# Kernel optimization log

Measured on AMD Instinct MI355X. Metric: run time of the kernel, lower is better.

Reference implementation:

```python
import jax, jax.numpy as jnp
import numpy as np

S, D, A, H, C = 2048, 256, 64, 8, 64  # seq_len, node_dim, num_aux, num_heads, num_channels
QUAT = 4
N_TYPES = 3  # nodes, aux, rot


def _linear_params(key, out_dim, in_dim, use_bias=True):
    kw, kb = jax.random.split(key)
    lim = 1.0 / np.sqrt(in_dim)
    W = jax.random.uniform(kw, (out_dim, in_dim), minval=-lim, maxval=lim, dtype=jnp.float32)
    if not use_bias:
        return W, None
    b = jax.random.uniform(kb, (out_dim,), minval=-lim, maxval=lim, dtype=jnp.float32)
    return W, b


def setup_inputs() -> dict:
    key = jax.random.key(0)
    ks = jax.random.split(key, 8)
    nodes = jax.random.normal(ks[0], (S, D), dtype=jnp.float32)
    aux = jax.random.normal(ks[1], (S, A), dtype=jnp.float32)
    rot = jax.random.normal(ks[2], (S, QUAT), dtype=jnp.float32)
    W_nodes, b_nodes = _linear_params(ks[3], H * C * 2, D)
    W_aux, b_aux = _linear_params(ks[4], H * C * 2, A)
    W_rot, _ = _linear_params(ks[5], H * C * 2, QUAT, use_bias=False)
    W_val, b_val = _linear_params(ks[6], D * H * N_TYPES, D)
    return {
        "nodes": nodes, "aux": aux, "rot": rot,
        "W_nodes": W_nodes, "b_nodes": b_nodes,
        "W_aux": W_aux, "b_aux": b_aux,
        "W_rot": W_rot,
        "W_val": W_val, "b_val": b_val,
    }


def reference(nodes, aux, rot, W_nodes, b_nodes, W_aux, b_aux, W_rot, W_val, b_val):
    seq_len = nodes.shape[0]
    # values: (S, 3H, D)
    val = (nodes @ W_val.T + b_val).reshape(seq_len, N_TYPES * H, -1)
    # per-source k/q: each (S, H, C)
    nodes_k, nodes_q = jnp.split((nodes @ W_nodes.T + b_nodes).reshape(seq_len, H, -1), 2, -1)
    aux_k, aux_q = jnp.split((aux @ W_aux.T + b_aux).reshape(seq_len, H, -1), 2, -1)
    rot_k, rot_q = jnp.split((rot @ W_rot.T).reshape(seq_len, H, -1), 2, -1)
    # concat along head axis -> (S, 3H, C)
    k = jnp.concatenate([nodes_k, aux_k, rot_k], axis=-2)
    q = jnp.concatenate([nodes_q, aux_q, rot_q], axis=-2)
    # (S, S, 3H) score tensor, scaled by 1/sqrt(num_heads) as in the original
    logits = jnp.einsum('ihc,jhc->ijh', k, q) / jnp.sqrt(jnp.asarray(H, nodes.dtype))
    att = jax.nn.softmax(logits, axis=-2)  # softmax over the j (key) axis
    out = jnp.einsum('ijh,jhd->id', att, val)  # (S, D)
    return out
```

## Files before the change

### kernel.cpp

```cpp
#include <hip/hip_runtime.h>

#define S_LEN 2048
#define NHEAD 24
#define CDIM 64
#define DDIM 256

typedef _Float16 f16x8 __attribute__((ext_vector_type(8)));
typedef float f32x4 __attribute__((ext_vector_type(4)));

__device__ __forceinline__ ushort f2h(float f) {
    _Float16 h = (_Float16)f;
    return __builtin_bit_cast(ushort, h);
}
__device__ __forceinline__ uint pkh(float a, float b) {
    auto v = __builtin_amdgcn_cvt_pkrtz(a, b);
    return __builtin_bit_cast(uint, v);
}
__device__ __forceinline__ uint pk2(float a, float b) {
    return (uint)f2h(a) | ((uint)f2h(b) << 16);
}

__device__ __forceinline__ int4 cvt8(const float* __restrict__ p) {
    float4 a = *(const float4*)p;
    float4 b = *(const float4*)(p + 4);
    f16x8 h;
    h[0] = (_Float16)a.x; h[1] = (_Float16)a.y;
    h[2] = (_Float16)a.z; h[3] = (_Float16)a.w;
    h[4] = (_Float16)b.x; h[5] = (_Float16)b.y;
    h[6] = (_Float16)b.z; h[7] = (_Float16)b.w;
    return __builtin_bit_cast(int4, h);
}

#define SCALE_K 0.51006973f

__global__ __launch_bounds__(256) void prep_kernel(
    const float* __restrict__ nodes, const float* __restrict__ W_val,
    float* __restrict__ out, ushort* __restrict__ nodes16, ushort* __restrict__ Wval16)
{
    int idx = blockIdx.x * 256 + threadIdx.x;
    if (idx < 131072) {
        ((float4*)out)[idx] = float4{0.f, 0.f, 0.f, 0.f};
    } else if (idx < 196608) {
        int i = idx - 131072;
        *(int4*)&nodes16[i * 8] = cvt8(&nodes[i * 8]);
    } else {
        int i = idx - 196608;
        *(int4*)&Wval16[i * 8] = cvt8(&W_val[i * 8]);
    }
}

__global__ __launch_bounds__(256) void proj_kernel(
    const float* __restrict__ nodes, const float* __restrict__ W_nodes,
    const float* __restrict__ b_nodes,
    const float* __restrict__ aux, const float* __restrict__ W_aux,
    const float* __restrict__ b_aux,
    const float* __restrict__ rot, const float* __restrict__ W_rot,
    const ushort* __restrict__ nodes16, const ushort* __restrict__ Wval16,
    const float* __restrict__ b_val,
    ushort* __restrict__ Kbuf, ushort* __restrict__ Qbuf, ushort* __restrict__ Vt)
{
    __shared__ ushort Asub[128 * 72];
    __shared__ ushort Wsub[128 * 72];
    const int blk = blockIdx.x;
    const int tid = threadIdx.x;
    const int wave = tid >> 6, lane = tid & 63;
    const int g = lane >> 4, c = lane & 15;

    if (blk < 768) {
        const int wm = wave & 1, wn = wave >> 1;
        const int m0 = (blk / 48) * 128, n0 = (blk % 48) * 128;
        const int K = 256;

        f32x4 acc[16];
#pragma unroll
        for (int t = 0; t < 16; t++) acc[t] = f32x4{0, 0, 0, 0};

        for (int k0 = 0; k0 < K; k0 += 64) {
            __syncthreads();
#pragma unroll
            for (int q = 0; q < 4; q++) {
                int i = tid + 256 * q;
                int row = i >> 3, kc = (i & 7) * 8;
                *(int4*)&Asub[row * 72 + kc] = *(const int4*)&nodes16[(m0 + row) * K + k0 + kc];
                *(int4*)&Wsub[row * 72 + kc] = *(const int4*)&Wval16[(n0 + row) * K + k0 + kc];
            }
            __syncthreads();

            f16x8 af0[4], af1[4];
#pragma unroll
            for (int mt = 0; mt < 4; mt++) {
                const ushort* Ar = &Asub[(wm * 64 + mt * 16 + c) * 72 + g * 8];
                af0[mt] = *(const f16x8*)Ar;
                af1[mt] = *(const f16x8*)(Ar + 32);
            }
#pragma unroll
            for (int nt = 0; nt < 4; nt++) {
                const ushort* Wr = &Wsub[(wn * 64 + nt * 16 + c) * 72 + g * 8];
                f16x8 bf0 = *(const f16x8*)Wr;
                f16x8 bf1 = *(const f16x8*)(Wr + 32);
#pragma unroll
                for (int mt = 0; mt < 4; mt++) {
                    acc[mt * 4 + nt] = __builtin_amdgcn_mfma_f32_16x16x32_f16(af0[mt], bf0, acc[mt * 4 + nt], 0, 0, 0);
                    acc[mt * 4 + nt] = __builtin_amdgcn_mfma_f32_16x16x32_f16(af1[mt], bf1, acc[mt * 4 + nt], 0, 0, 0);
                }
            }
        }

#pragma unroll
        for (int nt = 0; nt < 4; nt++) {
            int n = n0 + wn * 64 + nt * 16 + c;
            float bv = b_val[n];
            int h = n >> 8, d = n & 255;
#pragma unroll
            for (int mt = 0; mt < 4; mt++) {
                int m = m0 + wm * 64 + mt * 16 + g * 4;
                f32x4 v = acc[mt * 4 + nt];
                uint2 pw;
                pw.x = pk2(v[0] + bv, v[1] + bv);
                pw.y = pk2(v[2] + bv, v[3] + bv);
                *(uint2*)&Vt[(h * DDIM + d) * S_LEN + m] = pw;
            }
        }
    } else if (blk < 1792) {
        const int sub = blk - 768;
        const float *A, *W, *b;
        int K, hbase;
        if (sub < 512) { A = nodes; W = W_nodes; b = b_nodes; K = 256; hbase = 0; }
        else           { A = aux;   W = W_aux;   b = b_aux;   K = 64;  hbase = 8; }
        const int t5 = sub & 511;
        const int m0 = (t5 >> 4) * 64, n0 = (t5 & 15) * 64;
        const int srow = tid >> 2;
        const int skk = (tid & 3) * 8;

        f32x4 acc[4] = {f32x4{0,0,0,0}, f32x4{0,0,0,0}, f32x4{0,0,0,0}, f32x4{0,0,0,0}};

        for (int k0 = 0; k0 < K; k0 += 32) {
            __syncthreads();
            *(int4*)&Asub[srow * 40 + skk] = cvt8(&A[(m0 + srow) * K + k0 + skk]);
            *(int4*)&Wsub[srow * 40 + skk] = cvt8(&W[(n0 + srow) * K + k0 + skk]);
            __syncthreads();
            f16x8 af = *(const f16x8*)&Asub[(wave * 16 + c) * 40 + g * 8];
#pragma unroll
            for (int t = 0; t < 4; t++) {
                f16x8 bf = *(const f16x8*)&Wsub[(t * 16 + c) * 40 + g * 8];
                acc[t] = __builtin_amdgcn_mfma_f32_16x16x32_f16(af, bf, acc[t], 0, 0, 0);
            }
        }

#pragma unroll
        for (int t = 0; t < 4; t++) {
            int n = n0 + t * 16 + c;
            float bv = b[n];
            int h = hbase + (n >> 7);
            int cc = n & 127;
            float sc = (cc < 64) ? SCALE_K : 1.0f;
#pragma unroll
            for (int r = 0; r < 4; r++) {
                int m = m0 + wave * 16 + g * 4 + r;
                ushort u = f2h((acc[t][r] + bv) * sc);
                if (cc < 64) Kbuf[(h * S_LEN + m) * CDIM + cc] = u;
                else         Qbuf[(h * S_LEN + m) * CDIM + cc - 64] = u;
            }
        }
    } else {
        int u = (blk - 1792) * 256 + tid;
        int i = u >> 7;
        int n8 = (u & 127) * 8;
        int cc = n8 & 127;
        float sc = (cc < 64) ? SCALE_K : 1.0f;
        float4 r = *(const float4*)&rot[i * 4];
        ushort pv[8];
#pragma unroll
        for (int q = 0; q < 8; q++) {
            float4 w = *(const float4*)&W_rot[(n8 + q) * 4];
            pv[q] = f2h((r.x * w.x + r.y * w.y + r.z * w.z + r.w * w.w) * sc);
        }
        int h = 16 + (n8 >> 7);
        int4 pkt = *(int4*)pv;
        if (cc < 64) *(int4*)&Kbuf[(h * S_LEN + i) * CDIM + cc] = pkt;
        else         *(int4*)&Qbuf[(h * S_LEN + i) * CDIM + cc - 64] = pkt;
    }
}

__global__ __launch_bounds__(256, 3) void flash_kernel(
    const ushort* __restrict__ Kbuf, const ushort* __restrict__ Qbuf,
    const ushort* __restrict__ Vt, float* __restrict__ out)
{
    __shared__ ushort Qlds[2][64 * 72];
    __shared__ ushort Plds[2][64 * 72];
    __shared__ float  Alds[2][64];
    __shared__ int    Need[2][4] __attribute__((aligned(16)));

    const int tid = threadIdx.x;
    const int wave = tid >> 6, lane = tid & 63;
    const int g = lane >> 4, c = lane & 15;
    const int lin = blockIdx.y * 32 + blockIdx.x;
    const int xcd = lin & 7;
    const int slot = lin >> 3;
    const int h = xcd * 3 + (slot >> 5);
    const int i0 = (slot & 31) * 64;
    const float THR = 8.0f;

    const ushort* Krow = &Kbuf[(h * S_LEN + i0 + wave * 16 + c) * CDIM + g * 8];
    f16x8 ka0 = *(const f16x8*)Krow;
    f16x8 ka1 = *(const f16x8*)(Krow + 32);

    const ushort* Vbase = &Vt[(h * DDIM + wave * 64 + c) * S_LEN + g * 8];
    const ushort* Qh = &Qbuf[h * S_LEN * CDIM];

    const int qr0 = tid >> 3, qc0 = (tid & 7) * 8;
    const int qr1 = qr0 + 32;

    *(int4*)&Qlds[0][qr0 * 72 + qc0] = *(const int4*)&Qh[qr0 * CDIM + qc0];
    *(int4*)&Qlds[0][qr1 * 72 + qc0] = *(const int4*)&Qh[qr1 * CDIM + qc0];
    int4 qn0 = *(const int4*)&Qh[(64 + qr0) * CDIM + qc0];
    int4 qn1 = *(const int4*)&Qh[(64 + qr1) * CDIM + qc0];

    f16x8 vf0[4], vf1[4];
#pragma unroll
    for (int u = 0; u < 4; u++) {
        const ushort* Vr = Vbase + (u * 16) * S_LEN;
        vf0[u] = *(const f16x8*)Vr;
        vf1[u] = *(const f16x8*)(Vr + 32);
    }

    f32x4 acc[16];
#pragma unroll
    for (int u = 0; u < 16; u++) acc[u] = f32x4{0, 0, 0, 0};
    float mrow = -1e30f, lrow = 0.f;

    __syncthreads();

    {
        f32x4 Sf[4];
#pragma unroll
        for (int jc = 0; jc < 4; jc++) {
            const ushort* Qr = &Qlds[0][(jc * 16 + c) * 72 + g * 8];
            f16x8 qb0 = *(const f16x8*)Qr;
            f16x8 qb1 = *(const f16x8*)(Qr + 32);
            f32x4 s = {0, 0, 0, 0};
            s = __builtin_amdgcn_mfma_f32_16x16x32_f16(qb0, ka0, s, 0, 0, 0);
            s = __builtin_amdgcn_mfma_f32_16x16x32_f16(qb1, ka1, s, 0, 0, 0);
            Sf[jc] = s;
        }
        float tm = -1e30f;
#pragma unroll
        for (int jc = 0; jc < 4; jc++)
            tm = fmaxf(tm, fmaxf(fmaxf(Sf[jc][0], Sf[jc][1]),
                                 fmaxf(Sf[jc][2], Sf[jc][3])));
        tm = fmaxf(tm, __shfl_xor(tm, 16));
        tm = fmaxf(tm, __shfl_xor(tm, 32));
        const bool need = __any(tm > mrow + THR);
        float nm, alpha;
        if (need) { nm = fmaxf(tm, mrow); alpha = exp2f(mrow - nm); }
        else      { nm = mrow; alpha = 1.0f; }
        if (lane == 0) Need[0][wave] = need ? 1 : 0;
        float rs = 0.f;
#pragma unroll
        for (int jc = 0; jc < 4; jc++) {
            float p0 = exp2f(Sf[jc][0] - nm);
            float p1 = exp2f(Sf[jc][1] - nm);
            float p2 = exp2f(Sf[jc][2] - nm);
            float p3 = exp2f(Sf[jc][3] - nm);
            rs += (p0 + p1) + (p2 + p3);
            uint2 w;
            w.x = pkh(p0, p1);
            w.y = pkh(p2, p3);
            *(uint2*)&Plds[0][(wave * 16 + c) * 72 + jc * 16 + g * 4] = w;
        }
        lrow = lrow * alpha + rs;
        mrow = nm;
        if (g == 0) Alds[0][wave * 16 + c] = alpha;
    }
    *(int4*)&Qlds[1][qr0 * 72 + qc0] = qn0;
    *(int4*)&Qlds[1][qr1 * 72 + qc0] = qn1;

    for (int t = 0; t < 31; ++t) {
        const int cur = t & 1, nxt = cur ^ 1;
        __syncthreads();

        if (t < 30) {
            qn0 = *(const int4*)&Qh[((t + 2) * 64 + qr0) * CDIM + qc0];
            qn1 = *(const int4*)&Qh[((t + 2) * 64 + qr1) * CDIM + qc0];
        }

        f32x4 Sf[4];
#pragma unroll
        for (int jc = 0; jc < 4; jc++) {
            const ushort* Qr = &Qlds[nxt][(jc * 16 + c) * 72 + g * 8];
            f16x8 qb0 = *(const f16x8*)Qr;
            f16x8 qb1 = *(const f16x8*)(Qr + 32);
            f32x4 s = {0, 0, 0, 0};
            s = __builtin_amdgcn_mfma_f32_16x16x32_f16(qb0, ka0, s, 0, 0, 0);
            s = __builtin_amdgcn_mfma_f32_16x16x32_f16(qb1, ka1, s, 0, 0, 0);
            Sf[jc] = s;
        }

        int4 nf = *(const int4*)&Need[cur][0];
        if (nf.x | nf.y | nf.z | nf.w) {
#pragma unroll
            for (int b = 0; b < 4; b++) {
                f32x4 ab = *(const f32x4*)&Alds[cur][b * 16 + g * 4];
#pragma unroll
                for (int u = 0; u < 4; u++) acc[b * 4 + u] *= ab;
            }
        }

#pragma unroll
        for (int b = 0; b < 4; b++) {
            const ushort* Pr = &Plds[cur][(b * 16 + c) * 72 + g * 8];
            f16x8 pa0 = *(const f16x8*)Pr;
            f16x8 pa1 = *(const f16x8*)(Pr + 32);
#pragma unroll
            for (int u = 0; u < 4; u++) {
                acc[b * 4 + u] = __builtin_amdgcn_mfma_f32_16x16x32_f16(pa0, vf0[u], acc[b * 4 + u], 0, 0, 0);
                acc[b * 4 + u] = __builtin_amdgcn_mfma_f32_16x16x32_f16(pa1, vf1[u], acc[b * 4 + u], 0, 0, 0);
            }
        }

#pragma unroll
        for (int u = 0; u < 4; u++) {
            const ushort* Vr = Vbase + (u * 16) * S_LEN + (t + 1) * 64;
            vf0[u] = *(const f16x8*)Vr;
            vf1[u] = *(const f16x8*)(Vr + 32);
        }

        {
            float tl = -1e30f;
#pragma unroll
            for (int jc = 0; jc < 4; jc++)
                tl = fmaxf(tl, fmaxf(fmaxf(Sf[jc][0], Sf[jc][1]),
                                     fmaxf(Sf[jc][2], Sf[jc][3])));
            const bool need = __any(tl > mrow + THR);
            float nm, alpha;
            if (need) {
                float tm = fmaxf(tl, __shfl_xor(tl, 16));
                tm = fmaxf(tm, __shfl_xor(tm, 32));
                nm = fmaxf(tm, mrow);
                alpha = exp2f(mrow - nm);
            } else { nm = mrow; alpha = 1.0f; }
            if (lane == 0) Need[nxt][wave] = need ? 1 : 0;
            float rs = 0.f;
#pragma unroll
            for (int jc = 0; jc < 4; jc++) {
                float p0 = exp2f(Sf[jc][0] - nm);
                float p1 = exp2f(Sf[jc][1] - nm);
                float p2 = exp2f(Sf[jc][2] - nm);
                float p3 = exp2f(Sf[jc][3] - nm);
                rs += (p0 + p1) + (p2 + p3);
                uint2 w;
                w.x = pkh(p0, p1);
                w.y = pkh(p2, p3);
                *(uint2*)&Plds[nxt][(wave * 16 + c) * 72 + jc * 16 + g * 4] = w;
            }
            lrow = lrow * alpha + rs;
            mrow = nm;
            if (g == 0) Alds[nxt][wave * 16 + c] = alpha;
        }

        if (t < 30) {
            *(int4*)&Qlds[cur][qr0 * 72 + qc0] = qn0;
            *(int4*)&Qlds[cur][qr1 * 72 + qc0] = qn1;
        }
    }

    __syncthreads();
    {
        int4 nf = *(const int4*)&Need[1][0];
        if (nf.x | nf.y | nf.z | nf.w) {
#pragma unroll
            for (int b = 0; b < 4; b++) {
                f32x4 ab = *(const f32x4*)&Alds[1][b * 16 + g * 4];
#pragma unroll
                for (int u = 0; u < 4; u++) acc[b * 4 + u] *= ab;
            }
        }
#pragma unroll
        for (int b = 0; b < 4; b++) {
            const ushort* Pr = &Plds[1][(b * 16 + c) * 72 + g * 8];
            f16x8 pa0 = *(const f16x8*)Pr;
            f16x8 pa1 = *(const f16x8*)(Pr + 32);
#pragma unroll
            for (int u = 0; u < 4; u++) {
                acc[b * 4 + u] = __builtin_amdgcn_mfma_f32_16x16x32_f16(pa0, vf0[u], acc[b * 4 + u], 0, 0, 0);
                acc[b * 4 + u] = __builtin_amdgcn_mfma_f32_16x16x32_f16(pa1, vf1[u], acc[b * 4 + u], 0, 0, 0);
            }
        }
    }

    lrow += __shfl_xor(lrow, 16);
    lrow += __shfl_xor(lrow, 32);

    __syncthreads();
    if (g == 0) Alds[0][wave * 16 + c] = 1.0f / lrow;
    __syncthreads();
#pragma unroll
    for (int b = 0; b < 4; b++) {
        f32x4 lb = *(const f32x4*)&Alds[0][b * 16 + g * 4];
#pragma unroll
        for (int u = 0; u < 4; u++)
#pragma unroll
            for (int r = 0; r < 4; r++) {
                int i = i0 + b * 16 + g * 4 + r;
                int d = wave * 64 + u * 16 + c;
                atomicAdd(&out[i * DDIM + d], acc[b * 4 + u][r] * lb[r]);
            }
    }
}

extern "C" void kernel_launch(void* const* d_in, const int* in_sizes, int n_in,
                              void* d_out, int out_size, void* d_ws, size_t ws_size,
                              hipStream_t stream) {
    const float *nodes = 0, *aux = 0, *rot = 0, *W_nodes = 0, *b_nodes = 0,
                *W_aux = 0, *b_aux = 0, *W_rot = 0, *W_val = 0, *b_val = 0;
    int i1024[2] = {-1, -1};
    int n1024 = 0;
    for (int i = 0; i < n_in; ++i) {
        const float* p = (const float*)d_in[i];
        switch (in_sizes[i]) {
            case 524288:  nodes   = p; break;
            case 131072:  aux     = p; break;
            case 8192:    rot     = p; break;
            case 262144:  W_nodes = p; break;
            case 65536:   W_aux   = p; break;
            case 4096:    W_rot   = p; break;
            case 1572864: W_val   = p; break;
            case 6144:    b_val   = p; break;
            case 1024:    if (n1024 < 2) i1024[n1024] = i; n1024++; break;
            default: break;
        }
    }
    if (n1024 == 2) {
        b_nodes = (const float*)d_in[i1024[0]];
        b_aux   = (const float*)d_in[i1024[1]];
    }
    if (!nodes || !aux || !rot || !W_nodes || !b_nodes || !W_aux || !b_aux ||
        !W_rot || !W_val || !b_val) {
        nodes   = (const float*)d_in[0];
        aux     = (const float*)d_in[1];
        rot     = (const float*)d_in[2];
        W_nodes = (const float*)d_in[3];
        b_nodes = (const float*)d_in[4];
        W_aux   = (const float*)d_in[5];
        b_aux   = (const float*)d_in[6];
        W_rot   = (const float*)d_in[7];
        W_val   = (const float*)d_in[8];
        b_val   = (const float*)d_in[9];
    }
    float* out = (float*)d_out;

    float*  Opad = (float*)d_ws;
    ushort* Kbuf = (ushort*)(Opad + S_LEN * DDIM);
    ushort* Qbuf = Kbuf + NHEAD * S_LEN * CDIM;
    ushort* Vt   = Qbuf + NHEAD * S_LEN * CDIM;
    ushort* nodes16 = Vt + NHEAD * DDIM * S_LEN;
    ushort* Wval16  = nodes16 + 524288;

    dim3 blk(256);
    prep_kernel<<<dim3(1536), blk, 0, stream>>>(nodes, W_val, out, nodes16, Wval16);
    proj_kernel<<<dim3(2816), blk, 0, stream>>>(
        nodes, W_nodes, b_nodes, aux, W_aux, b_aux, rot, W_rot,
        nodes16, Wval16, b_val, Kbuf, Qbuf, Vt);
    flash_kernel<<<dim3(32, NHEAD), blk, 0, stream>>>(Kbuf, Qbuf, Vt, out);
}
```

Baseline: 241.5 us.

## Load projection GEMM tiles directly to LDS with XOR swizzle; raise MFMA priority

The value-projection GEMM now stages A and W tiles through global_load_lds with an XOR-swizzled 64-wide row layout. This replaces register round-trip loads into padded 72-wide LDS rows and aims to cut VGPR traffic and bank conflicts. The attention loop also wraps its MFMA sections in s_setprio(1)/s_setprio(0), so waves issuing matrix ops get scheduling priority. The direct-to-LDS path depends on the per-lane address-to-LDS layout matching the swizzle, and the priority hints may give little benefit.

```diff
diff --git a/kernel.cpp b/kernel.cpp
--- a/kernel.cpp
+++ b/kernel.cpp
@@ -29,6 +29,12 @@
     h[4] = (_Float16)b.x; h[5] = (_Float16)b.y;
     h[6] = (_Float16)b.z; h[7] = (_Float16)b.w;
     return __builtin_bit_cast(int4, h);
+}
+
+__device__ __forceinline__ void gload16(const void* g, void* l) {
+    __builtin_amdgcn_global_load_lds(
+        (const __attribute__((address_space(1))) void*)g,
+        (__attribute__((address_space(3))) void*)l, 16, 0, 0);
 }
 
 #define SCALE_K 0.51006973f
@@ -70,6 +76,7 @@
         const int wm = wave & 1, wn = wave >> 1;
         const int m0 = (blk / 48) * 128, n0 = (blk % 48) * 128;
         const int K = 256;
+        const int x = c & 7;
 
         f32x4 acc[16];
 #pragma unroll
@@ -79,25 +86,27 @@
             __syncthreads();
 #pragma unroll
             for (int q = 0; q < 4; q++) {
-                int i = tid + 256 * q;
-                int row = i >> 3, kc = (i & 7) * 8;
-                *(int4*)&Asub[row * 72 + kc] = *(const int4*)&nodes16[(m0 + row) * K + k0 + kc];
-                *(int4*)&Wsub[row * 72 + kc] = *(const int4*)&Wval16[(n0 + row) * K + k0 + kc];
+                const int r0 = wave * 32 + q * 8;
+                const int row = r0 + (lane >> 3);
+                const int sl = lane & 7;
+                const int sc = ((sl ^ (row & 7)) * 8);
+                gload16(&nodes16[(m0 + row) * K + k0 + sc], &Asub[r0 * 64]);
+                gload16(&Wval16[(n0 + row) * K + k0 + sc], &Wsub[r0 * 64]);
             }
             __syncthreads();
 
             f16x8 af0[4], af1[4];
 #pragma unroll
             for (int mt = 0; mt < 4; mt++) {
-                const ushort* Ar = &Asub[(wm * 64 + mt * 16 + c) * 72 + g * 8];
-                af0[mt] = *(const f16x8*)Ar;
-                af1[mt] = *(const f16x8*)(Ar + 32);
+                const int row = wm * 64 + mt * 16 + c;
+                af0[mt] = *(const f16x8*)&Asub[row * 64 + ((g ^ x) * 8)];
+                af1[mt] = *(const f16x8*)&Asub[row * 64 + (((g + 4) ^ x) * 8)];
             }
 #pragma unroll
             for (int nt = 0; nt < 4; nt++) {
-                const ushort* Wr = &Wsub[(wn * 64 + nt * 16 + c) * 72 + g * 8];
-                f16x8 bf0 = *(const f16x8*)Wr;
-                f16x8 bf1 = *(const f16x8*)(Wr + 32);
+                const int row = wn * 64 + nt * 16 + c;
+                f16x8 bf0 = *(const f16x8*)&Wsub[row * 64 + ((g ^ x) * 8)];
+                f16x8 bf1 = *(const f16x8*)&Wsub[row * 64 + (((g + 4) ^ x) * 8)];
 #pragma unroll
                 for (int mt = 0; mt < 4; mt++) {
                     acc[mt * 4 + nt] = __builtin_amdgcn_mfma_f32_16x16x32_f16(af0[mt], bf0, acc[mt * 4 + nt], 0, 0, 0);
@@ -285,6 +294,7 @@
         }
 
         f32x4 Sf[4];
+        __builtin_amdgcn_s_setprio(1);
 #pragma unroll
         for (int jc = 0; jc < 4; jc++) {
             const ushort* Qr = &Qlds[nxt][(jc * 16 + c) * 72 + g * 8];
@@ -295,6 +305,7 @@
             s = __builtin_amdgcn_mfma_f32_16x16x32_f16(qb1, ka1, s, 0, 0, 0);
             Sf[jc] = s;
         }
+        __builtin_amdgcn_s_setprio(0);
 
         int4 nf = *(const int4*)&Need[cur][0];
         if (nf.x | nf.y | nf.z | nf.w) {
@@ -306,6 +317,7 @@
             }
         }
 
+        __builtin_amdgcn_s_setprio(1);
 #pragma unroll
         for (int b = 0; b < 4; b++) {
             const ushort* Pr = &Plds[cur][(b * 16 + c) * 72 + g * 8];
@@ -317,6 +329,7 @@
                 acc[b * 4 + u] = __builtin_amdgcn_mfma_f32_16x16x32_f16(pa1, vf1[u], acc[b * 4 + u], 0, 0, 0);
             }
         }
+        __builtin_amdgcn_s_setprio(0);
 
 #pragma unroll
         for (int u = 0; u < 4; u++) {
```

Result: no change. 238.0 us (-1.4%).
